# Optimization experiments

Measured on AMD Instinct MI355X. Metric: run time of the kernel, lower is better.

Reference implementation:

```python
import jax, jax.numpy as jnp
import numpy as np

B, S, D, H = 64, 256, 2048, 8
DH = D // H  # 256; NOTE: S must equal DH for the original module's broadcast to be valid
EPS = 1e-06


def setup_inputs() -> dict:
    key = jax.random.key(0)
    ks = jax.random.split(key, 8)
    s = 1.0 / np.sqrt(D)
    x = jax.random.normal(ks[0], (B, S, D), jnp.float32)
    Wq = jax.random.normal(ks[1], (D, D), jnp.float32) * s
    Wk = jax.random.normal(ks[2], (D, D), jnp.float32) * s
    Wv = jax.random.normal(ks[3], (D, D), jnp.float32) * s
    Wo = jax.random.normal(ks[4], (2 * D, D), jnp.float32) * (1.0 / np.sqrt(2 * D))
    bq = jnp.zeros((D,), jnp.float32)
    bk = jnp.zeros((D,), jnp.float32)
    bv = jnp.zeros((D,), jnp.float32)
    bo = jnp.zeros((D,), jnp.float32)
    gamma = jnp.ones((D,), jnp.float32)
    beta = jnp.zeros((D,), jnp.float32)
    return {"x": x, "Wq": Wq, "bq": bq, "Wk": Wk, "bk": bk, "Wv": Wv, "bv": bv,
            "Wo": Wo, "bo": bo, "gamma": gamma, "beta": beta}


def reference(x, Wq, bq, Wk, bk, Wv, bv, Wo, bo, gamma, beta):
    def split_heads(t):  # [B,S,D] -> [B,H,S,DH]
        return t.reshape(B, S, H, DH).transpose(0, 2, 1, 3)

    q_proj = x @ Wq + bq  # reused later as the residual projection
    q = jax.nn.elu(split_heads(q_proj)) + 1.0
    k = jax.nn.elu(split_heads(x @ Wk + bk)) + 1.0
    v = split_heads(x @ Wv + bv)

    key_sum = k.sum(axis=2, keepdims=True)  # [B,H,1,DH]
    # Original TF code broadcasts [B,H,S,S] / [B,H,1,DH]; valid because S == DH
    scores = jnp.einsum('bhqd,bhkd->bhqk', q, k) / (key_sum + EPS)
    attn = jnp.einsum('bhqk,bhkd->bhqd', scores, v)
    attn = attn.transpose(0, 2, 1, 3).reshape(B, S, D)

    summary = jnp.broadcast_to(attn.mean(axis=1, keepdims=True), (B, S, D))
    combined = jnp.concatenate([attn, summary], axis=-1) @ Wo + bo  # [B,S,D]
    # dropout is identity (training=False)

    z = q_proj + combined
    mu = z.mean(axis=-1, keepdims=True)
    var = z.var(axis=-1, keepdims=True)
    return (z - mu) / jnp.sqrt(var + EPS) * gamma + beta
```

## Files before the change

kernel.cpp:

```cpp
#include <hip/hip_runtime.h>
#include <hip/hip_bf16.h>

typedef __attribute__((ext_vector_type(8))) __bf16 bf16x8v;
typedef __attribute__((ext_vector_type(4))) float f32x4;
typedef __attribute__((ext_vector_type(4))) unsigned short u16x4;
typedef __attribute__((ext_vector_type(8))) unsigned short u16x8;

#define LN_EPS 1e-6f

__device__ __forceinline__ unsigned short f2bf(float f) {
  union { float f; unsigned int u; } v; v.f = f;
  unsigned int r = v.u + 0x7fffu + ((v.u >> 16) & 1u);
  return (unsigned short)(r >> 16);
}
__device__ __forceinline__ float bf2f(unsigned short u) {
  union { unsigned int u; float f; } v; v.u = ((unsigned int)u) << 16;
  return v.f;
}
__device__ __forceinline__ float elu1(float x) {
  return x > 0.f ? x + 1.f : __expf(x);
}
__device__ __forceinline__ void gload16(const void* g, void* l) {
  __builtin_amdgcn_global_load_lds((__attribute__((address_space(1))) void*)g,
                                   (__attribute__((address_space(3))) void*)l,
                                   16, 0, 0);
}

__global__ __launch_bounds__(256) void cvt_f32_bf16(const float* __restrict__ in,
                                                    unsigned short* __restrict__ out, long n) {
  long stride = (long)gridDim.x * 256 * 8;
  for (long i = ((long)blockIdx.x * 256 + threadIdx.x) * 8; i < n; i += stride) {
    float4 a = *(const float4*)(in + i);
    float4 b = *(const float4*)(in + i + 4);
    u16x8 o;
    o[0] = f2bf(a.x); o[1] = f2bf(a.y); o[2] = f2bf(a.z); o[3] = f2bf(a.w);
    o[4] = f2bf(b.x); o[5] = f2bf(b.y); o[6] = f2bf(b.z); o[7] = f2bf(b.w);
    *(u16x8*)(out + i) = o;
  }
}

__global__ __launch_bounds__(256) void tr_cvt(const float* __restrict__ in,
                                              unsigned short* __restrict__ out, int R, int C) {
  __shared__ float t[64][65];
  int r0 = blockIdx.y * 64, c0 = blockIdx.x * 64;
  for (int idx = threadIdx.x; idx < 4096; idx += 256) {
    int r = idx >> 6, c = idx & 63;
    t[r][c] = in[(long)(r0 + r) * C + c0 + c];
  }
  __syncthreads();
  for (int idx = threadIdx.x; idx < 4096; idx += 256) {
    int c = idx >> 6, r = idx & 63;
    out[(long)(c0 + c) * R + r0 + r] = f2bf(t[r][c]);
  }
}

__global__ __launch_bounds__(256) void colsum_bf16(const unsigned short* __restrict__ in,
                                                   float* __restrict__ out, int rows, float scale) {
  int b = blockIdx.y;
  int col = blockIdx.x * 256 + threadIdx.x;
  const unsigned short* p = in + (long)b * rows * 2048 + col;
  float acc = 0.f;
  for (int s = 0; s < rows; ++s) acc += bf2f(p[(long)s * 2048]);
  out[(long)b * 2048 + col] = acc * scale;
}

__global__ __launch_bounds__(256) void srow_part(const float* __restrict__ summ,
                                                 const float* __restrict__ Wo2,
                                                 float* __restrict__ part) {
  int col = blockIdx.x * 256 + threadIdx.x;
  int b = blockIdx.y;
  int k0 = blockIdx.z * 256;
  const float* s = summ + (long)b * 2048 + k0;
  const float* w = Wo2 + (long)k0 * 2048 + col;
  float acc = 0.f;
#pragma unroll 8
  for (int k = 0; k < 256; ++k) acc += s[k] * w[(long)k * 2048];
  part[((long)blockIdx.z * 64 + b) * 2048 + col] = acc;
}
__global__ __launch_bounds__(256) void srow_sum(const float* __restrict__ part,
                                                float* __restrict__ srow) {
  int col = blockIdx.x * 256 + threadIdx.x;
  int b = blockIdx.y;
  float acc = 0.f;
#pragma unroll
  for (int kb = 0; kb < 8; ++kb) acc += part[((long)kb * 64 + b) * 2048 + col];
  srow[(long)b * 2048 + col] = acc;
}

__global__ __launch_bounds__(256) void ln_k(const float* __restrict__ z,
                                            const float* __restrict__ gamma,
                                            const float* __restrict__ beta,
                                            float* __restrict__ out) {
  long row = blockIdx.x;
  const float* zr = z + row * 2048;
  int t = threadIdx.x;
  float4 a = *(const float4*)(zr + t * 4);
  float4 b = *(const float4*)(zr + 1024 + t * 4);
  float s = a.x + a.y + a.z + a.w + b.x + b.y + b.z + b.w;
  float q = a.x * a.x + a.y * a.y + a.z * a.z + a.w * a.w +
            b.x * b.x + b.y * b.y + b.z * b.z + b.w * b.w;
#pragma unroll
  for (int o = 32; o >= 1; o >>= 1) { s += __shfl_xor(s, o); q += __shfl_xor(q, o); }
  __shared__ float ss[4], qq[4];
  if ((t & 63) == 0) { ss[t >> 6] = s; qq[t >> 6] = q; }
  __syncthreads();
  s = ss[0] + ss[1] + ss[2] + ss[3];
  q = qq[0] + qq[1] + qq[2] + qq[3];
  float mu = s * (1.f / 2048.f);
  float var = q * (1.f / 2048.f) - mu * mu;
  float rstd = rsqrtf(var + LN_EPS);
  float4 g1 = *(const float4*)(gamma + t * 4);
  float4 b1 = *(const float4*)(beta + t * 4);
  float4 g2 = *(const float4*)(gamma + 1024 + t * 4);
  float4 b2 = *(const float4*)(beta + 1024 + t * 4);
  float4 o1, o2;
  o1.x = (a.x - mu) * rstd * g1.x + b1.x;
  o1.y = (a.y - mu) * rstd * g1.y + b1.y;
  o1.z = (a.z - mu) * rstd * g1.z + b1.z;
  o1.w = (a.w - mu) * rstd * g1.w + b1.w;
  o2.x = (b.x - mu) * rstd * g2.x + b2.x;
  o2.y = (b.y - mu) * rstd * g2.y + b2.y;
  o2.z = (b.z - mu) * rstd * g2.z + b2.z;
  o2.w = (b.w - mu) * rstd * g2.w + b2.w;
  *(float4*)(out + row * 2048 + t * 4) = o1;
  *(float4*)(out + row * 2048 + 1024 + t * 4) = o2;
}

struct GemmArgs {
  const unsigned short* A; long lda, sAb, sAh;
  const unsigned short* B; long ldb, sBb, sBh;
  char* C; long ldc, sCb, sCh;
  int K;
  const float* aux; long sXb, sXh;
  const float* resid;
  const float* srow;
  unsigned short* out2;
};

template <int EPI>
__device__ __forceinline__ void epi_frag(const GemmArgs& g, char* Cb, int bz, int hz,
                                         long grow0, long gcol, f32x4 v) {
  if (EPI == 0) {
    const float bias = g.aux[gcol];
    float* Cf = (float*)Cb;
#pragma unroll
    for (int rr = 0; rr < 4; ++rr) {
      const long idx = (grow0 + rr) * g.ldc + gcol;
      const float vv = v[rr] + bias;
      Cf[idx] = vv;
      g.out2[idx] = f2bf(elu1(vv));
    }
  } else if (EPI == 1) {
    const float bias = g.aux[gcol];
    unsigned short* Ch = (unsigned short*)Cb;
#pragma unroll
    for (int rr = 0; rr < 4; ++rr)
      Ch[(grow0 + rr) * g.ldc + gcol] = f2bf(elu1(v[rr] + bias));
  } else if (EPI == 2) {
    const float bias = g.aux[gcol];
    unsigned short* Ch = (unsigned short*)Cb;
    const long batch = grow0 >> 8;
    const int sloc = (int)(grow0 & 255);
    u16x4 pk;
#pragma unroll
    for (int rr = 0; rr < 4; ++rr) pk[rr] = f2bf(v[rr] + bias);
    *(u16x4*)(Ch + (batch * 2048 + gcol) * 256 + sloc) = pk;
  } else if (EPI == 3) {
    const float* divs = g.aux + bz * g.sXb + hz * g.sXh;
    const float d = divs[gcol] + LN_EPS;
    unsigned short* Ch = (unsigned short*)Cb;
#pragma unroll
    for (int rr = 0; rr < 4; ++rr)
      Ch[(grow0 + rr) * g.ldc + gcol] = f2bf(v[rr] / d);
  } else if (EPI == 4) {
    unsigned short* Ch = (unsigned short*)Cb;
#pragma unroll
    for (int rr = 0; rr < 4; ++rr)
      Ch[(grow0 + rr) * g.ldc + gcol] = f2bf(v[rr]);
  } else {
    const float bias = g.aux[gcol];
    float* Cf = (float*)Cb;
#pragma unroll
    for (int rr = 0; rr < 4; ++rr) {
      const long grow = grow0 + rr;
      const long idx = grow * g.ldc + gcol;
      Cf[idx] = v[rr] + bias + g.resid[idx] + g.srow[(grow >> 8) * 2048 + gcol];
    }
  }
}

template <int EPI>
__global__ __launch_bounds__(256, 4) void gemm_bt(GemmArgs g) {
  const int tid = threadIdx.x;
  const int lane = tid & 63;
  const int wave = tid >> 6;
  const int wm = wave >> 1, wn = wave & 1;
  const int bz = (int)blockIdx.z >> 3, hz = (int)blockIdx.z & 7;
  const long mBase = (long)blockIdx.x * 128;
  const long nBase = (long)blockIdx.y * 128;
  const unsigned short* Ab = g.A + bz * g.sAb + hz * g.sAh;
  const unsigned short* Bb = g.B + bz * g.sBb + hz * g.sBh;

  __shared__ __align__(16) unsigned short Asm[128 * 64];
  __shared__ __align__(16) unsigned short Bsm[128 * 64];

  f32x4 acc[4][4] = {};

  for (int kt = 0; kt < g.K; kt += 64) {
#pragma unroll
    for (int i = 0; i < 4; ++i) {
      const int u = i * 256 + tid;
      const int rr = u >> 3;
      const int cc = (((u & 7) ^ (rr & 7)) << 3);
      gload16(Ab + (mBase + rr) * g.lda + kt + cc, Asm + (size_t)u * 8);
      gload16(Bb + (nBase + rr) * g.ldb + kt + cc, Bsm + (size_t)u * 8);
    }
    __syncthreads();
#pragma unroll
    for (int ks = 0; ks < 64; ks += 32) {
      const int kof = ks + ((lane >> 4) << 3);
      bf16x8v a[4], b[4];
#pragma unroll
      for (int mi = 0; mi < 4; ++mi) {
        const int row = wm * 64 + mi * 16 + (lane & 15);
        a[mi] = *(const bf16x8v*)&Asm[row * 64 + (kof ^ ((row & 7) << 3))];
      }
#pragma unroll
      for (int ni = 0; ni < 4; ++ni) {
        const int row = wn * 64 + ni * 16 + (lane & 15);
        b[ni] = *(const bf16x8v*)&Bsm[row * 64 + (kof ^ ((row & 7) << 3))];
      }
#pragma unroll
      for (int mi = 0; mi < 4; ++mi)
#pragma unroll
        for (int ni = 0; ni < 4; ++ni)
          acc[mi][ni] = __builtin_amdgcn_mfma_f32_16x16x32_bf16(a[mi], b[ni], acc[mi][ni], 0, 0, 0);
    }
    __syncthreads();
  }

  char* Cb = g.C + bz * g.sCb + hz * g.sCh;
#pragma unroll
  for (int mi = 0; mi < 4; ++mi) {
    const long grow0 = mBase + wm * 64 + mi * 16 + ((lane >> 4) << 2);
#pragma unroll
    for (int ni = 0; ni < 4; ++ni)
      epi_frag<EPI>(g, Cb, bz, hz, grow0, nBase + wn * 64 + ni * 16 + (lane & 15), acc[mi][ni]);
  }
}

extern "C" void kernel_launch(void* const* d_in, const int* in_sizes, int n_in,
                              void* d_out, int out_size, void* d_ws, size_t ws_size,
                              hipStream_t stream) {
  (void)in_sizes; (void)n_in; (void)out_size;
  const float* x     = (const float*)d_in[0];
  const float* Wq    = (const float*)d_in[1];
  const float* bq    = (const float*)d_in[2];
  const float* Wk    = (const float*)d_in[3];
  const float* bk    = (const float*)d_in[4];
  const float* Wv    = (const float*)d_in[5];
  const float* bv    = (const float*)d_in[6];
  const float* Wo    = (const float*)d_in[7];
  const float* bo    = (const float*)d_in[8];
  const float* gamma = (const float*)d_in[9];
  const float* beta  = (const float*)d_in[10];
  float* out = (float*)d_out;

  const long M = 16384, D = 2048;
  char* ws = (char*)d_ws;
  size_t o = 0;
  unsigned short* xbf = (unsigned short*)(ws + o); o += (size_t)M * D * 2;
  unsigned short* wqT = (unsigned short*)(ws + o); o += (size_t)D * D * 2;
  unsigned short* wkT = (unsigned short*)(ws + o); o += (size_t)D * D * 2;
  unsigned short* wvT = (unsigned short*)(ws + o); o += (size_t)D * D * 2;
  unsigned short* woT = (unsigned short*)(ws + o); o += (size_t)D * D * 2;
  float*          qpro = (float*)(ws + o);         o += (size_t)M * D * 4;
  unsigned short* qact = (unsigned short*)(ws + o); o += (size_t)M * D * 2;
  unsigned short* kact = (unsigned short*)(ws + o); o += (size_t)M * D * 2;
  unsigned short* vT   = (unsigned short*)(ws + o); o += (size_t)M * D * 2;
  unsigned short* P    = (unsigned short*)(ws + o); o += (size_t)512 * 65536 * 2;
  float* ksum = (float*)(ws + o); o += (size_t)64 * 2048 * 4;
  float* summ = (float*)(ws + o); o += (size_t)64 * 2048 * 4;
  float* srow = (float*)(ws + o); o += (size_t)64 * 2048 * 4;
  unsigned short* attn = xbf;
  float* spart = (float*)P;
  if (ws_size < o) return;

  cvt_f32_bf16<<<2048, 256, 0, stream>>>(x, xbf, M * D);
  tr_cvt<<<dim3(32, 32), 256, 0, stream>>>(Wq, wqT, 2048, 2048);
  tr_cvt<<<dim3(32, 32), 256, 0, stream>>>(Wk, wkT, 2048, 2048);
  tr_cvt<<<dim3(32, 32), 256, 0, stream>>>(Wv, wvT, 2048, 2048);
  tr_cvt<<<dim3(32, 32), 256, 0, stream>>>(Wo, woT, 2048, 2048);

  GemmArgs a{};
  a.A = xbf; a.lda = 2048; a.sAb = 0; a.sAh = 0;
  a.B = wqT; a.ldb = 2048; a.sBb = 0; a.sBh = 0;
  a.C = (char*)qpro; a.ldc = 2048; a.sCb = 0; a.sCh = 0;
  a.K = 2048; a.aux = bq; a.sXb = 0; a.sXh = 0;
  a.resid = nullptr; a.srow = nullptr; a.out2 = qact;
  gemm_bt<0><<<dim3(128, 16, 1), 256, 0, stream>>>(a);

  a.B = wkT; a.C = (char*)kact; a.aux = bk; a.out2 = nullptr;
  gemm_bt<1><<<dim3(128, 16, 1), 256, 0, stream>>>(a);

  a.B = wvT; a.C = (char*)vT; a.aux = bv;
  gemm_bt<2><<<dim3(128, 16, 1), 256, 0, stream>>>(a);

  colsum_bf16<<<dim3(8, 64), 256, 0, stream>>>(kact, ksum, 256, 1.0f);

  GemmArgs sA{};
  sA.A = qact; sA.lda = 2048; sA.sAb = 256 * 2048; sA.sAh = 256;
  sA.B = kact; sA.ldb = 2048; sA.sBb = 256 * 2048; sA.sBh = 256;
  sA.C = (char*)P; sA.ldc = 256; sA.sCb = 8L * 65536 * 2; sA.sCh = 65536L * 2;
  sA.K = 256; sA.aux = ksum; sA.sXb = 2048; sA.sXh = 256;
  sA.resid = nullptr; sA.srow = nullptr; sA.out2 = nullptr;
  gemm_bt<3><<<dim3(2, 2, 512), 256, 0, stream>>>(sA);

  GemmArgs tA{};
  tA.A = P; tA.lda = 256; tA.sAb = 8L * 65536; tA.sAh = 65536;
  tA.B = vT; tA.ldb = 256; tA.sBb = 2048L * 256; tA.sBh = 256 * 256;
  tA.C = (char*)attn; tA.ldc = 2048; tA.sCb = 256L * 2048 * 2; tA.sCh = 256 * 2;
  tA.K = 256; tA.aux = nullptr; tA.sXb = 0; tA.sXh = 0;
  tA.resid = nullptr; tA.srow = nullptr; tA.out2 = nullptr;
  gemm_bt<4><<<dim3(2, 2, 512), 256, 0, stream>>>(tA);

  colsum_bf16<<<dim3(8, 64), 256, 0, stream>>>(attn, summ, 256, 1.0f / 256.0f);
  srow_part<<<dim3(8, 64, 8), 256, 0, stream>>>(summ, Wo + (size_t)2048 * 2048, spart);
  srow_sum<<<dim3(8, 64), 256, 0, stream>>>(spart, srow);

  GemmArgs zA{};
  zA.A = attn; zA.lda = 2048; zA.sAb = 0; zA.sAh = 0;
  zA.B = woT; zA.ldb = 2048; zA.sBb = 0; zA.sBh = 0;
  zA.C = (char*)qpro; zA.ldc = 2048; zA.sCb = 0; zA.sCh = 0;
  zA.K = 2048; zA.aux = bo; zA.sXb = 0; zA.sXh = 0;
  zA.resid = qpro; zA.srow = srow; zA.out2 = nullptr;
  gemm_bt<5><<<dim3(128, 16, 1), 256, 0, stream>>>(zA);

  ln_k<<<16384, 256, 0, stream>>>(qpro, gamma, beta, out);
}
```

Before: 1.084 ms.

## Fuse Q/K/V projections into one GEMM launch and store pre-norm activations as bf16

The three separate Q, K and V projection GEMMs become one launch over a 48-wide N grid. This relies on the transposed weight buffers sitting back-to-back in the workspace, and the epilogue picks the output path from the column block. The q projection, used as residual and as the pre-LayerNorm sum, is now stored as bf16 instead of fp32. That halves the memory traffic for its write in the first GEMM, its read-modify-write in the output GEMM, and the LayerNorm read. The trade-off is extra rounding of the residual and of the LayerNorm input, which could affect accuracy.

```diff
diff --git a/kernel.cpp b/kernel.cpp
--- a/kernel.cpp
+++ b/kernel.cpp
@@ -87,18 +87,21 @@
   srow[(long)b * 2048 + col] = acc;
 }
 
-__global__ __launch_bounds__(256) void ln_k(const float* __restrict__ z,
+__global__ __launch_bounds__(256) void ln_k(const unsigned short* __restrict__ z,
                                             const float* __restrict__ gamma,
                                             const float* __restrict__ beta,
                                             float* __restrict__ out) {
   long row = blockIdx.x;
-  const float* zr = z + row * 2048;
   int t = threadIdx.x;
-  float4 a = *(const float4*)(zr + t * 4);
-  float4 b = *(const float4*)(zr + 1024 + t * 4);
-  float s = a.x + a.y + a.z + a.w + b.x + b.y + b.z + b.w;
-  float q = a.x * a.x + a.y * a.y + a.z * a.z + a.w * a.w +
-            b.x * b.x + b.y * b.y + b.z * b.z + b.w * b.w;
+  u16x8 zv = *(const u16x8*)(z + row * 2048 + t * 8);
+  float zf[8];
+  float s = 0.f, q = 0.f;
+#pragma unroll
+  for (int j = 0; j < 8; ++j) {
+    zf[j] = bf2f(zv[j]);
+    s += zf[j];
+    q += zf[j] * zf[j];
+  }
 #pragma unroll
   for (int o = 32; o >= 1; o >>= 1) { s += __shfl_xor(s, o); q += __shfl_xor(q, o); }
   __shared__ float ss[4], qq[4];
@@ -109,21 +112,21 @@
   float mu = s * (1.f / 2048.f);
   float var = q * (1.f / 2048.f) - mu * mu;
   float rstd = rsqrtf(var + LN_EPS);
-  float4 g1 = *(const float4*)(gamma + t * 4);
-  float4 b1 = *(const float4*)(beta + t * 4);
-  float4 g2 = *(const float4*)(gamma + 1024 + t * 4);
-  float4 b2 = *(const float4*)(beta + 1024 + t * 4);
+  float4 g1 = *(const float4*)(gamma + t * 8);
+  float4 g2 = *(const float4*)(gamma + t * 8 + 4);
+  float4 b1 = *(const float4*)(beta + t * 8);
+  float4 b2 = *(const float4*)(beta + t * 8 + 4);
   float4 o1, o2;
-  o1.x = (a.x - mu) * rstd * g1.x + b1.x;
-  o1.y = (a.y - mu) * rstd * g1.y + b1.y;
-  o1.z = (a.z - mu) * rstd * g1.z + b1.z;
-  o1.w = (a.w - mu) * rstd * g1.w + b1.w;
-  o2.x = (b.x - mu) * rstd * g2.x + b2.x;
-  o2.y = (b.y - mu) * rstd * g2.y + b2.y;
-  o2.z = (b.z - mu) * rstd * g2.z + b2.z;
-  o2.w = (b.w - mu) * rstd * g2.w + b2.w;
-  *(float4*)(out + row * 2048 + t * 4) = o1;
-  *(float4*)(out + row * 2048 + 1024 + t * 4) = o2;
+  o1.x = (zf[0] - mu) * rstd * g1.x + b1.x;
+  o1.y = (zf[1] - mu) * rstd * g1.y + b1.y;
+  o1.z = (zf[2] - mu) * rstd * g1.z + b1.z;
+  o1.w = (zf[3] - mu) * rstd * g1.w + b1.w;
+  o2.x = (zf[4] - mu) * rstd * g2.x + b2.x;
+  o2.y = (zf[5] - mu) * rstd * g2.y + b2.y;
+  o2.z = (zf[6] - mu) * rstd * g2.z + b2.z;
+  o2.w = (zf[7] - mu) * rstd * g2.w + b2.w;
+  *(float4*)(out + row * 2048 + t * 8) = o1;
+  *(float4*)(out + row * 2048 + t * 8 + 4) = o2;
 }
 
 struct GemmArgs {
@@ -132,39 +135,45 @@
   char* C; long ldc, sCb, sCh;
   int K;
   const float* aux; long sXb, sXh;
-  const float* resid;
+  const unsigned short* residb;
   const float* srow;
   unsigned short* out2;
+  const float* bk2;
+  const float* bv2;
+  unsigned short* kact2;
+  unsigned short* vt2;
 };
 
 template <int EPI>
 __device__ __forceinline__ void epi_frag(const GemmArgs& g, char* Cb, int bz, int hz,
                                          long grow0, long gcol, f32x4 v) {
-  if (EPI == 0) {
-    const float bias = g.aux[gcol];
-    float* Cf = (float*)Cb;
-#pragma unroll
-    for (int rr = 0; rr < 4; ++rr) {
-      const long idx = (grow0 + rr) * g.ldc + gcol;
-      const float vv = v[rr] + bias;
-      Cf[idx] = vv;
-      g.out2[idx] = f2bf(elu1(vv));
+  if (EPI == 6) {
+    const int wsel = (int)(gcol >> 11);
+    const long cw = gcol & 2047;
+    if (wsel == 0) {
+      const float bias = g.aux[cw];
+      unsigned short* Ch = (unsigned short*)Cb;
+#pragma unroll
+      for (int rr = 0; rr < 4; ++rr) {
+        const long idx = (grow0 + rr) * 2048 + cw;
+        const float vv = v[rr] + bias;
+        Ch[idx] = f2bf(vv);
+        g.out2[idx] = f2bf(elu1(vv));
+      }
+    } else if (wsel == 1) {
+      const float bias = g.bk2[cw];
+#pragma unroll
+      for (int rr = 0; rr < 4; ++rr)
+        g.kact2[(grow0 + rr) * 2048 + cw] = f2bf(elu1(v[rr] + bias));
+    } else {
+      const float bias = g.bv2[cw];
+      const long batch = grow0 >> 8;
+      const int sloc = (int)(grow0 & 255);
+      u16x4 pk;
+#pragma unroll
+      for (int rr = 0; rr < 4; ++rr) pk[rr] = f2bf(v[rr] + bias);
+      *(u16x4*)(g.vt2 + (batch * 2048 + cw) * 256 + sloc) = pk;
     }
-  } else if (EPI == 1) {
-    const float bias = g.aux[gcol];
-    unsigned short* Ch = (unsigned short*)Cb;
-#pragma unroll
-    for (int rr = 0; rr < 4; ++rr)
-      Ch[(grow0 + rr) * g.ldc + gcol] = f2bf(elu1(v[rr] + bias));
-  } else if (EPI == 2) {
-    const float bias = g.aux[gcol];
-    unsigned short* Ch = (unsigned short*)Cb;
-    const long batch = grow0 >> 8;
-    const int sloc = (int)(grow0 & 255);
-    u16x4 pk;
-#pragma unroll
-    for (int rr = 0; rr < 4; ++rr) pk[rr] = f2bf(v[rr] + bias);
-    *(u16x4*)(Ch + (batch * 2048 + gcol) * 256 + sloc) = pk;
   } else if (EPI == 3) {
     const float* divs = g.aux + bz * g.sXb + hz * g.sXh;
     const float d = divs[gcol] + LN_EPS;
@@ -179,12 +188,13 @@
       Ch[(grow0 + rr) * g.ldc + gcol] = f2bf(v[rr]);
   } else {
     const float bias = g.aux[gcol];
-    float* Cf = (float*)Cb;
+    unsigned short* Ch = (unsigned short*)Cb;
 #pragma unroll
     for (int rr = 0; rr < 4; ++rr) {
       const long grow = grow0 + rr;
       const long idx = grow * g.ldc + gcol;
-      Cf[idx] = v[rr] + bias + g.resid[idx] + g.srow[(grow >> 8) * 2048 + gcol];
+      const float vv = v[rr] + bias + bf2f(g.residb[idx]) + g.srow[(grow >> 8) * 2048 + gcol];
+      Ch[idx] = f2bf(vv);
     }
   }
 }
@@ -274,7 +284,7 @@
   unsigned short* wkT = (unsigned short*)(ws + o); o += (size_t)D * D * 2;
   unsigned short* wvT = (unsigned short*)(ws + o); o += (size_t)D * D * 2;
   unsigned short* woT = (unsigned short*)(ws + o); o += (size_t)D * D * 2;
-  float*          qpro = (float*)(ws + o);         o += (size_t)M * D * 4;
+  unsigned short* qpro = (unsigned short*)(ws + o); o += (size_t)M * D * 2;
   unsigned short* qact = (unsigned short*)(ws + o); o += (size_t)M * D * 2;
   unsigned short* kact = (unsigned short*)(ws + o); o += (size_t)M * D * 2;
   unsigned short* vT   = (unsigned short*)(ws + o); o += (size_t)M * D * 2;
@@ -297,14 +307,9 @@
   a.B = wqT; a.ldb = 2048; a.sBb = 0; a.sBh = 0;
   a.C = (char*)qpro; a.ldc = 2048; a.sCb = 0; a.sCh = 0;
   a.K = 2048; a.aux = bq; a.sXb = 0; a.sXh = 0;
-  a.resid = nullptr; a.srow = nullptr; a.out2 = qact;
-  gemm_bt<0><<<dim3(128, 16, 1), 256, 0, stream>>>(a);
-
-  a.B = wkT; a.C = (char*)kact; a.aux = bk; a.out2 = nullptr;
-  gemm_bt<1><<<dim3(128, 16, 1), 256, 0, stream>>>(a);
-
-  a.B = wvT; a.C = (char*)vT; a.aux = bv;
-  gemm_bt<2><<<dim3(128, 16, 1), 256, 0, stream>>>(a);
+  a.residb = nullptr; a.srow = nullptr; a.out2 = qact;
+  a.bk2 = bk; a.bv2 = bv; a.kact2 = kact; a.vt2 = vT;
+  gemm_bt<6><<<dim3(128, 48, 1), 256, 0, stream>>>(a);
 
   colsum_bf16<<<dim3(8, 64), 256, 0, stream>>>(kact, ksum, 256, 1.0f);
 
@@ -313,7 +318,7 @@
   sA.B = kact; sA.ldb = 2048; sA.sBb = 256 * 2048; sA.sBh = 256;
   sA.C = (char*)P; sA.ldc = 256; sA.sCb = 8L * 65536 * 2; sA.sCh = 65536L * 2;
   sA.K = 256; sA.aux = ksum; sA.sXb = 2048; sA.sXh = 256;
-  sA.resid = nullptr; sA.srow = nullptr; sA.out2 = nullptr;
+  sA.residb = nullptr; sA.srow = nullptr; sA.out2 = nullptr;
   gemm_bt<3><<<dim3(2, 2, 512), 256, 0, stream>>>(sA);
 
   GemmArgs tA{};
@@ -321,7 +326,7 @@
   tA.B = vT; tA.ldb = 256; tA.sBb = 2048L * 256; tA.sBh = 256 * 256;
   tA.C = (char*)attn; tA.ldc = 2048; tA.sCb = 256L * 2048 * 2; tA.sCh = 256 * 2;
   tA.K = 256; tA.aux = nullptr; tA.sXb = 0; tA.sXh = 0;
-  tA.resid = nullptr; tA.srow = nullptr; tA.out2 = nullptr;
+  tA.residb = nullptr; tA.srow = nullptr; tA.out2 = nullptr;
   gemm_bt<4><<<dim3(2, 2, 512), 256, 0, stream>>>(tA);
 
   colsum_bf16<<<dim3(8, 64), 256, 0, stream>>>(attn, summ, 256, 1.0f / 256.0f);
@@ -333,7 +338,7 @@
   zA.B = woT; zA.ldb = 2048; zA.sBb = 0; zA.sBh = 0;
   zA.C = (char*)qpro; zA.ldc = 2048; zA.sCb = 0; zA.sCh = 0;
   zA.K = 2048; zA.aux = bo; zA.sXb = 0; zA.sXh = 0;
-  zA.resid = qpro; zA.srow = srow; zA.out2 = nullptr;
+  zA.residb = qpro; zA.srow = srow; zA.out2 = nullptr;
   gemm_bt<5><<<dim3(128, 16, 1), 256, 0, stream>>>(zA);
 
   ln_k<<<16384, 256, 0, stream>>>(qpro, gamma, beta, out);
```

New measurement: 1.043 ms. 3.8% less time.
